# Kernel optimization log

Measured on AMD Instinct MI355X. Metric: run time of the kernel, lower is better.

Reference implementation:

```python
import jax, jax.numpy as jnp
import numpy as np

FIELD_DIMS = [100000, 1000, 100, 50]
NUM_FEATURES = 12
NUM_CAT = len(FIELD_DIMS)
NUM_CONT = NUM_FEATURES - NUM_CAT
D = 32            # embed_dim
HID = [64, 32]
B, T = 1024, 200
BN_EPS = 1e-5


def setup_inputs() -> dict:
    key = jax.random.key(0)
    ks = jax.random.split(key, 32)
    # x: [B, T, F]; first NUM_CAT cols are integer category ids stored as float
    cat_cols = [jax.random.randint(ks[i], (B, T, 1), 0, FIELD_DIMS[i]).astype(jnp.float32)
                for i in range(NUM_CAT)]
    cont_cols = jax.random.normal(ks[4], (B, T, NUM_CONT), dtype=jnp.float32)
    x = jnp.concatenate(cat_cols + [cont_cols], axis=-1)
    s = 0.05
    inp = {"x": x}
    for i, fd in enumerate(FIELD_DIMS):
        inp[f"emb{i}"] = jax.random.normal(ks[5 + i], (fd, D), dtype=jnp.float32) * s
        inp[f"lin{i}"] = jax.random.normal(ks[9 + i], (fd, D), dtype=jnp.float32) * s
    # Conv1d(1, D, 1) per continuous field == per-field affine map scalar -> D
    inp["cont_w"]  = jax.random.normal(ks[13], (NUM_CONT, D), dtype=jnp.float32) * s
    inp["cont_b"]  = jax.random.normal(ks[14], (NUM_CONT, D), dtype=jnp.float32) * s
    inp["clin_w"]  = jax.random.normal(ks[15], (NUM_CONT, D), dtype=jnp.float32) * s
    inp["clin_b"]  = jax.random.normal(ks[16], (NUM_CONT, D), dtype=jnp.float32) * s
    inp["fin_bias"] = jnp.zeros((D,), dtype=jnp.float32)
    # DNN tower: kernel_size-1 Conv1d == dense over channel dim
    dims = [NUM_FEATURES * D] + HID
    for li in range(len(HID)):
        fan_in = dims[li]
        inp[f"w{li+1}"] = jax.random.normal(ks[17 + 4 * li], (HID[li], fan_in), dtype=jnp.float32) / np.sqrt(fan_in)
        inp[f"b{li+1}"] = jnp.zeros((HID[li],), dtype=jnp.float32)
        inp[f"g{li+1}"] = jnp.ones((HID[li],), dtype=jnp.float32)
        inp[f"beta{li+1}"] = jnp.zeros((HID[li],), dtype=jnp.float32)
    inp["w_out"] = jax.random.normal(ks[30], (D, HID[-1]), dtype=jnp.float32) / np.sqrt(HID[-1])
    inp["b_out"] = jnp.zeros((D,), dtype=jnp.float32)
    return inp


def _batchnorm(h, g, b):
    # training-mode BN over (batch, time), biased variance (torch default)
    mu = h.mean(axis=(0, 1))
    var = h.var(axis=(0, 1))
    return g * (h - mu) * jax.lax.rsqrt(var + BN_EPS) + b


def reference(x, emb0, emb1, emb2, emb3, lin0, lin1, lin2, lin3,
              cont_w, cont_b, clin_w, clin_b, fin_bias,
              w1, b1, g1, beta1, w2, b2, g2, beta2, w_out, b_out):
    embs = [emb0, emb1, emb2, emb3]
    lins = [lin0, lin1, lin2, lin3]
    cat_idx = x[..., :NUM_CAT].astype(jnp.int32)          # [B,T,C]
    xc = x[..., NUM_CAT:]                                  # [B,T,Nc]

    # per-field embeddings -> [B,T,F,D]
    cat_emb = jnp.stack([embs[i][cat_idx[..., i]] for i in range(NUM_CAT)], axis=2)
    cont_emb = xc[..., None] * cont_w + cont_b             # [B,T,Nc,D]
    emb_all = jnp.concatenate([cat_emb, cont_emb], axis=2)  # [B,T,F,D]

    # FM pairwise interaction (sum-of-squares trick)
    s = emb_all.sum(axis=2)                                # [B,T,D]
    interaction = 0.5 * (s * s - (emb_all * emb_all).sum(axis=2))

    # linear terms
    lin_cat = sum(lins[i][cat_idx[..., i]] for i in range(NUM_CAT))      # [B,T,D]
    lin_cont = (xc[..., None] * clin_w + clin_b).sum(axis=2)             # [B,T,D]
    linear = lin_cat + lin_cont + fin_bias

    # DNN tower (k=1 convs == dense over F*D channels); dropout omitted (eval)
    h = emb_all.reshape(B, T, NUM_FEATURES * D)
    h = jax.nn.relu(_batchnorm(h @ w1.T + b1, g1, beta1))
    h = jax.nn.relu(_batchnorm(h @ w2.T + b2, g2, beta2))
    dnn = h @ w_out.T + b_out                              # [B,T,D]

    return linear + interaction + dnn                      # [B,T,D]
```

## Files before the change

kernel.cpp:

```cpp
#include <hip/hip_runtime.h>
#include <hip/hip_bf16.h>

typedef __hip_bfloat16 bf16;

#define ROWS 204800
#define N_INV (1.0f / 204800.0f)

__device__ float g_stats[256];
__device__ bf16  g_E1_0b[100000 * 64];
__device__ float g_E1_1[1000 * 64];
__device__ float g_E1_2[100 * 64];
__device__ float g_E1_3[50 * 64];
__device__ float g_U[8 * 64];
__device__ float g_Vb[64];
__device__ bf16  g_h1p[ROWS * 64];
__device__ bf16  g_h2p[ROWS * 32];
__device__ bf16  g_fmp[ROWS * 32];

__device__ __forceinline__ int clampi(int v, int hi) {
    return v < 0 ? 0 : (v > hi ? hi : v);
}
__device__ __forceinline__ float rl_f(float v, int l) {
    return __uint_as_float((unsigned int)__builtin_amdgcn_readlane((int)__float_as_uint(v), l));
}
__device__ __forceinline__ float us2f(unsigned short u) {
    return __uint_as_float(((unsigned int)u) << 16);
}

__global__ __launch_bounds__(64) void precompute_kernel(
    const float* __restrict__ emb1, const float* __restrict__ emb2, const float* __restrict__ emb3,
    const float* __restrict__ cont_w, const float* __restrict__ cont_b,
    const float* __restrict__ w1, const float* __restrict__ b1)
{
    int b = blockIdx.x;
    int k = threadIdx.x;
    __shared__ float row[32];

    if (b < 1150) {
        const float* tab; float* out; int i, colOff;
        if (b < 1000)      { tab = emb1; out = g_E1_1; i = b;        colOff = 32; }
        else if (b < 1100) { tab = emb2; out = g_E1_2; i = b - 1000; colOff = 64; }
        else               { tab = emb3; out = g_E1_3; i = b - 1100; colOff = 96; }
        if (k < 32) row[k] = tab[i * 32 + k];
        __syncthreads();
        const float* wr = w1 + k * 384 + colOff;
        float acc = 0.f;
        #pragma unroll
        for (int d = 0; d < 32; ++d) acc = fmaf(row[d], wr[d], acc);
        out[i * 64 + k] = acc;
    } else {
        g_stats[k]       = 0.f;
        g_stats[k + 64]  = 0.f;
        g_stats[k + 128] = 0.f;
        g_stats[k + 192] = 0.f;

        float vb = b1[k];
        #pragma unroll
        for (int j = 0; j < 8; ++j) {
            const float* wr = w1 + k * 384 + (4 + j) * 32;
            float u = 0.f;
            #pragma unroll
            for (int d = 0; d < 32; ++d) {
                float w = wr[d];
                u  = fmaf(cont_w[j * 32 + d], w, u);
                vb = fmaf(cont_b[j * 32 + d], w, vb);
            }
            g_U[j * 64 + k] = u;
        }
        g_Vb[k] = vb;
    }
}

__global__ __launch_bounds__(256) void e10_kernel(
    const float* __restrict__ emb0, const float* __restrict__ w1)
{
    int lane = threadIdx.x & 63;
    int wv   = threadIdx.x >> 6;
    int h    = lane >> 5;

    float w1col[32];
    {
        const float4* wr = (const float4*)(w1 + lane * 384);
        #pragma unroll
        for (int q = 0; q < 8; ++q) {
            float4 v = wr[q];
            w1col[4*q+0] = v.x; w1col[4*q+1] = v.y;
            w1col[4*q+2] = v.z; w1col[4*q+3] = v.w;
        }
    }

    for (int i = blockIdx.x * 8 + wv * 2; i < 100000; i += gridDim.x * 8) {
        int iA = i, iB = i + 1;
        float e = emb0[(h ? iB : iA) * 32 + (lane & 31)];

        float a0 = 0.f, a1 = 0.f, a2 = 0.f, a3 = 0.f;
        float b0 = 0.f, b1v = 0.f, b2v = 0.f, b3 = 0.f;
        #pragma unroll
        for (int dd = 0; dd < 32; dd += 4) {
            a0  = fmaf(rl_f(e, dd + 0),      w1col[dd + 0], a0);
            a1  = fmaf(rl_f(e, dd + 1),      w1col[dd + 1], a1);
            a2  = fmaf(rl_f(e, dd + 2),      w1col[dd + 2], a2);
            a3  = fmaf(rl_f(e, dd + 3),      w1col[dd + 3], a3);
            b0  = fmaf(rl_f(e, 32 + dd + 0), w1col[dd + 0], b0);
            b1v = fmaf(rl_f(e, 32 + dd + 1), w1col[dd + 1], b1v);
            b2v = fmaf(rl_f(e, 32 + dd + 2), w1col[dd + 2], b2v);
            b3  = fmaf(rl_f(e, 32 + dd + 3), w1col[dd + 3], b3);
        }
        g_E1_0b[iA * 64 + lane] = __float2bfloat16((a0 + a1) + (a2 + a3));
        g_E1_0b[iB * 64 + lane] = __float2bfloat16((b0 + b1v) + (b2v + b3));
    }
}

__global__ __launch_bounds__(256) void phase1_kernel(
    const float* __restrict__ x,
    const float* __restrict__ emb0, const float* __restrict__ lin0,
    const float* __restrict__ emb1, const float* __restrict__ lin1,
    const float* __restrict__ emb2, const float* __restrict__ lin2,
    const float* __restrict__ emb3, const float* __restrict__ lin3,
    const float* __restrict__ cont_w, const float* __restrict__ cont_b,
    const float* __restrict__ clin_w, const float* __restrict__ clin_b,
    const float* __restrict__ fin_bias)
{
    __shared__ float lsum[64], lsq[64];

    int tid  = threadIdx.x;
    int lane = tid & 63;
    int wv   = tid >> 6;
    int d    = lane & 31;
    bool lo  = lane < 32;

    if (tid < 64) { lsum[tid] = 0.f; lsq[tid] = 0.f; }
    __syncthreads();

    float uk[8];
    #pragma unroll
    for (int j = 0; j < 8; ++j) uk[j] = g_U[j * 64 + lane];
    float vbk = g_Vb[lane];

    float p1[8], p2[8], fb = 0.f;
    if (lo) {
        #pragma unroll
        for (int j = 0; j < 8; ++j) { p1[j] = cont_w[j * 32 + d]; p2[j] = cont_b[j * 32 + d]; }
    } else {
        #pragma unroll
        for (int j = 0; j < 8; ++j) { p1[j] = clin_w[j * 32 + d]; p2[j] = clin_b[j * 32 + d]; }
        fb = fin_bias[d];
    }

    const float* T0 = lo ? emb0 : lin0;
    const float* T1 = lo ? emb1 : lin1;
    const float* T2 = lo ? emb2 : lin2;
    const float* T3 = lo ? emb3 : lin3;

    int gw   = blockIdx.x * 4 + wv;
    int base = gw * 16;

    float xs[4];
    #pragma unroll
    for (int g = 0; g < 4; ++g)
        xs[g] = (lane < 48) ? x[(base + 4 * g) * 12 + lane] : 0.f;

    float ga[2][4], gb[2][4], gc[2][4], gd[2][4], t1[2][4], t2[2][4], t3[2][4];
    unsigned short e0u[2][4];

    auto issue = [&](int g, int s) {
        #pragma unroll
        for (int t = 0; t < 4; ++t) {
            int f  = t * 12;
            int i0 = clampi((int)rl_f(xs[g], f + 0), 99999);
            int i1 = clampi((int)rl_f(xs[g], f + 1), 999);
            int i2 = clampi((int)rl_f(xs[g], f + 2), 99);
            int i3 = clampi((int)rl_f(xs[g], f + 3), 49);
            ga[s][t]  = T0[i0 * 32 + d];
            gb[s][t]  = T1[i1 * 32 + d];
            gc[s][t]  = T2[i2 * 32 + d];
            gd[s][t]  = T3[i3 * 32 + d];
            e0u[s][t] = ((const unsigned short*)g_E1_0b)[i0 * 64 + lane];
            t1[s][t]  = g_E1_1[i1 * 64 + lane];
            t2[s][t]  = g_E1_2[i2 * 64 + lane];
            t3[s][t]  = g_E1_3[i3 * 64 + lane];
        }
    };

    issue(0, 0);

    float ss = 0.f, qq = 0.f;

    #pragma unroll
    for (int g = 0; g < 4; ++g) {
        int s = g & 1;
        if (g < 3) issue(g + 1, (g + 1) & 1);

        #pragma unroll
        for (int t = 0; t < 4; ++t) {
            int r  = base + 4 * g + t;
            int fo = t * 12 + 4;
            float xc[8];
            #pragma unroll
            for (int j = 0; j < 8; ++j) xc[j] = rl_f(xs[g], fo + j);

            float va = ga[s][t], vb = gb[s][t], vc = gc[s][t], vd = gd[s][t];

            float half_val;
            if (lo) {
                float s0 = va + vb, s1 = vc + vd;
                float q0 = fmaf(va, va, vb * vb);
                float q1 = fmaf(vc, vc, vd * vd);
                #pragma unroll
                for (int j = 0; j < 8; ++j) {
                    float ce = fmaf(xc[j], p1[j], p2[j]);
                    if (j & 1) { s1 += ce; q1 = fmaf(ce, ce, q1); }
                    else       { s0 += ce; q0 = fmaf(ce, ce, q0); }
                }
                float sfull = s0 + s1;
                half_val = 0.5f * (sfull * sfull - (q0 + q1));
            } else {
                float l0 = va + vb + fb, l1 = vc + vd;
                #pragma unroll
                for (int j = 0; j < 8; ++j) {
                    if (j & 1) l1 = fmaf(xc[j], p1[j], l1 + p2[j]);
                    else       l0 = fmaf(xc[j], p1[j], l0 + p2[j]);
                }
                half_val = l0 + l1;
            }
            float other = __shfl(half_val, lane | 32);
            if (lo) g_fmp[r * 32 + d] = __float2bfloat16(half_val + other);

            float h1 = ((vbk + us2f(e0u[s][t])) + (t1[s][t] + t2[s][t])) + t3[s][t];
            #pragma unroll
            for (int j = 0; j < 8; ++j) h1 = fmaf(xc[j], uk[j], h1);

            g_h1p[r * 64 + lane] = __float2bfloat16(h1);
            ss += h1;
            qq = fmaf(h1, h1, qq);
        }
    }

    atomicAdd(&lsum[lane], ss);
    atomicAdd(&lsq[lane], qq);
    __syncthreads();
    if (tid < 64) {
        atomicAdd(&g_stats[tid], lsum[tid]);
        atomicAdd(&g_stats[64 + tid], lsq[tid]);
    }
}

__global__ __launch_bounds__(256) void phase2_kernel(
    const float* __restrict__ w2, const float* __restrict__ b2,
    const float* __restrict__ g1, const float* __restrict__ beta1)
{
    __shared__ float sa[64], sc[64];
    __shared__ float ls[64];
    int tid  = threadIdx.x;
    if (tid < 64) {
        float mu  = g_stats[tid] * N_INV;
        float var = g_stats[64 + tid] * N_INV - mu * mu;
        float a   = g1[tid] * rsqrtf(var + 1e-5f);
        sa[tid] = a;
        sc[tid] = beta1[tid] - a * mu;
        ls[tid] = 0.f;
    }
    __syncthreads();

    int lane = tid & 63;
    int wv   = tid >> 6;
    size_t row = (size_t)(blockIdx.x * 4 + wv) * 64 + lane;

    const uint4* hrow = (const uint4*)(g_h1p + row * 64);

    float acc[32];
    #pragma unroll
    for (int m = 0; m < 32; ++m) acc[m] = 0.f;

    #pragma unroll
    for (int half = 0; half < 2; ++half) {
        uint4 u[4];
        #pragma unroll
        for (int q = 0; q < 4; ++q) u[q] = hrow[half * 4 + q];

        float y[32];
        #pragma unroll
        for (int q = 0; q < 4; ++q) {
            unsigned int w4[4] = {u[q].x, u[q].y, u[q].z, u[q].w};
            #pragma unroll
            for (int j = 0; j < 4; ++j) {
                int i  = q * 4 + j;
                int ch = half * 32 + 2 * i;
                float f0 = __uint_as_float(w4[j] << 16);
                float f1 = __uint_as_float(w4[j] & 0xffff0000u);
                y[2*i]     = fmaxf(0.f, fmaf(sa[ch],     f0, sc[ch]));
                y[2*i + 1] = fmaxf(0.f, fmaf(sa[ch + 1], f1, sc[ch + 1]));
            }
        }

        #pragma unroll
        for (int m = 0; m < 32; ++m) {
            const float* wr = w2 + m * 64 + half * 32;
            float a0 = 0.f, a1 = 0.f, a2 = 0.f, a3 = 0.f;
            #pragma unroll
            for (int k = 0; k < 32; k += 4) {
                a0 = fmaf(y[k + 0], wr[k + 0], a0);
                a1 = fmaf(y[k + 1], wr[k + 1], a1);
                a2 = fmaf(y[k + 2], wr[k + 2], a2);
                a3 = fmaf(y[k + 3], wr[k + 3], a3);
            }
            acc[m] += (a0 + a1) + (a2 + a3);
        }
    }

    #pragma unroll
    for (int m = 0; m < 32; ++m) acc[m] += b2[m];

    uint4 o[4];
    unsigned int* ow = (unsigned int*)o;
    #pragma unroll
    for (int i = 0; i < 16; ++i) {
        unsigned int lo16 = (unsigned int)__bfloat16_as_ushort(__float2bfloat16(acc[2*i]));
        unsigned int hi16 = (unsigned int)__bfloat16_as_ushort(__float2bfloat16(acc[2*i + 1]));
        ow[i] = lo16 | (hi16 << 16);
    }
    uint4* orow = (uint4*)(g_h2p + row * 32);
    #pragma unroll
    for (int q = 0; q < 4; ++q) orow[q] = o[q];

    #pragma unroll
    for (int c0 = 0; c0 < 32; c0 += 8) {
        float s[8], q[8];
        #pragma unroll
        for (int j = 0; j < 8; ++j) { s[j] = acc[c0 + j]; q[j] = s[j] * s[j]; }
        #pragma unroll
        for (int off = 32; off >= 1; off >>= 1) {
            #pragma unroll
            for (int j = 0; j < 8; ++j) {
                s[j] += __shfl_xor(s[j], off);
                q[j] += __shfl_xor(q[j], off);
            }
        }
        if (lane == 0) {
            #pragma unroll
            for (int j = 0; j < 8; ++j) {
                atomicAdd(&ls[c0 + j],      s[j]);
                atomicAdd(&ls[32 + c0 + j], q[j]);
            }
        }
    }
    __syncthreads();
    if (tid < 32)       atomicAdd(&g_stats[128 + tid], ls[tid]);
    else if (tid < 64)  atomicAdd(&g_stats[160 + (tid - 32)], ls[tid]);
}

__global__ __launch_bounds__(256) void phase3_kernel(
    const float* __restrict__ w_out, const float* __restrict__ b_out,
    const float* __restrict__ g2, const float* __restrict__ beta2,
    float* __restrict__ out)
{
    __shared__ float sa[32], sc[32];
    int tid  = threadIdx.x;
    if (tid < 32) {
        float mu  = g_stats[128 + tid] * N_INV;
        float var = g_stats[160 + tid] * N_INV - mu * mu;
        float a   = g2[tid] * rsqrtf(var + 1e-5f);
        sa[tid] = a;
        sc[tid] = beta2[tid] - a * mu;
    }
    __syncthreads();

    int lane = tid & 63;
    int wv   = tid >> 6;
    size_t row = (size_t)(blockIdx.x * 4 + wv) * 64 + lane;

    const uint4* hrow = (const uint4*)(g_h2p + row * 32);
    const uint4* frow = (const uint4*)(g_fmp + row * 32);
    uint4 u[4], fm4[4];
    #pragma unroll
    for (int q = 0; q < 4; ++q) { u[q] = hrow[q]; fm4[q] = frow[q]; }

    float y2[32];
    #pragma unroll
    for (int q = 0; q < 4; ++q) {
        unsigned int w4[4] = {u[q].x, u[q].y, u[q].z, u[q].w};
        #pragma unroll
        for (int j = 0; j < 4; ++j) {
            int i = q * 4 + j;
            float f0 = __uint_as_float(w4[j] << 16);
            float f1 = __uint_as_float(w4[j] & 0xffff0000u);
            y2[2*i]     = fmaxf(0.f, fmaf(sa[2*i],     f0, sc[2*i]));
            y2[2*i + 1] = fmaxf(0.f, fmaf(sa[2*i + 1], f1, sc[2*i + 1]));
        }
    }

    float fmv[32];
    {
        const unsigned int* fw = (const unsigned int*)fm4;
        #pragma unroll
        for (int i = 0; i < 16; ++i) {
            fmv[2*i]     = __uint_as_float(fw[i] << 16);
            fmv[2*i + 1] = __uint_as_float(fw[i] & 0xffff0000u);
        }
    }

    float res[32];
    #pragma unroll
    for (int dd = 0; dd < 32; ++dd) {
        const float* wr = w_out + dd * 32;
        float a0 = fmv[dd] + b_out[dd], a1 = 0.f, a2 = 0.f, a3 = 0.f;
        #pragma unroll
        for (int k = 0; k < 32; k += 4) {
            a0 = fmaf(y2[k + 0], wr[k + 0], a0);
            a1 = fmaf(y2[k + 1], wr[k + 1], a1);
            a2 = fmaf(y2[k + 2], wr[k + 2], a2);
            a3 = fmaf(y2[k + 3], wr[k + 3], a3);
        }
        res[dd] = (a0 + a1) + (a2 + a3);
    }

    float4* orow = (float4*)(out + row * 32);
    #pragma unroll
    for (int q = 0; q < 8; ++q)
        orow[q] = make_float4(res[4*q+0], res[4*q+1], res[4*q+2], res[4*q+3]);
}

extern "C" void kernel_launch(void* const* d_in, const int* in_sizes, int n_in,
                              void* d_out, int out_size, void* d_ws, size_t ws_size,
                              hipStream_t stream) {
    (void)in_sizes; (void)n_in; (void)out_size; (void)d_ws; (void)ws_size;

    const float* x       = (const float*)d_in[0];
    const float* emb0    = (const float*)d_in[1];
    const float* lin0    = (const float*)d_in[2];
    const float* emb1    = (const float*)d_in[3];
    const float* lin1    = (const float*)d_in[4];
    const float* emb2    = (const float*)d_in[5];
    const float* lin2    = (const float*)d_in[6];
    const float* emb3    = (const float*)d_in[7];
    const float* lin3    = (const float*)d_in[8];
    const float* cont_w  = (const float*)d_in[9];
    const float* cont_b  = (const float*)d_in[10];
    const float* clin_w  = (const float*)d_in[11];
    const float* clin_b  = (const float*)d_in[12];
    const float* fin_bias= (const float*)d_in[13];
    const float* w1      = (const float*)d_in[14];
    const float* b1      = (const float*)d_in[15];
    const float* g1      = (const float*)d_in[16];
    const float* beta1   = (const float*)d_in[17];
    const float* w2      = (const float*)d_in[18];
    const float* b2      = (const float*)d_in[19];
    const float* g2      = (const float*)d_in[20];
    const float* beta2   = (const float*)d_in[21];
    const float* w_out   = (const float*)d_in[22];
    const float* b_out   = (const float*)d_in[23];

    float* outp = (float*)d_out;

    hipLaunchKernelGGL(precompute_kernel, dim3(1151), dim3(64), 0, stream,
                       emb1, emb2, emb3, cont_w, cont_b, w1, b1);

    hipLaunchKernelGGL(e10_kernel, dim3(1600), dim3(256), 0, stream, emb0, w1);

    hipLaunchKernelGGL(phase1_kernel, dim3(3200), dim3(256), 0, stream,
                       x, emb0, lin0, emb1, lin1, emb2, lin2, emb3, lin3,
                       cont_w, cont_b, clin_w, clin_b, fin_bias);

    hipLaunchKernelGGL(phase2_kernel, dim3(800), dim3(256), 0, stream,
                       w2, b2, g1, beta1);

    hipLaunchKernelGGL(phase3_kernel, dim3(800), dim3(256), 0, stream,
                       w_out, b_out, g2, beta2, outp);
}
```

Baseline: 339.8 us.

## Stage phase2/phase3 row loads and stores through swizzled LDS for coalescing

Phase2 and phase3 previously had each lane read and write its own row with 16-byte strided accesses, which coalesce poorly across the wavefront. The kernels now use global_load_lds to bring each wave's 64-row tile into shared memory with an XOR swizzle that avoids bank conflicts. Outputs (h2 and the final result) are also staged through LDS, so global stores are contiguous across lanes. This costs extra LDS (32 KB per block), which can reduce occupancy. It also depends on hand-written waitcnt asm being correct, with no barrier between the wave-private LDS write and read.

```diff
diff --git a/kernel.cpp b/kernel.cpp
--- a/kernel.cpp
+++ b/kernel.cpp
@@ -26,6 +26,18 @@
 __device__ __forceinline__ float us2f(unsigned short u) {
     return __uint_as_float(((unsigned int)u) << 16);
 }
+
+__device__ __forceinline__ int swz8(int d) {
+    return (d & ~7) | ((d & 7) ^ ((d >> 3) & 7));
+}
+__device__ __forceinline__ int swz4(int d) {
+    return (d & ~3) | ((d & 3) ^ (((d >> 2) ^ (d >> 4)) & 3));
+}
+
+#define GLOAD16(gp, lp)                                                        \
+    __builtin_amdgcn_global_load_lds(                                          \
+        (const __attribute__((address_space(1))) unsigned int*)(gp),           \
+        (__attribute__((address_space(3))) unsigned int*)(lp), 16, 0, 0)
 
 __global__ __launch_bounds__(64) void precompute_kernel(
     const float* __restrict__ emb1, const float* __restrict__ emb2, const float* __restrict__ emb3,
@@ -251,7 +263,22 @@
 {
     __shared__ float sa[64], sc[64];
     __shared__ float ls[64];
+    __shared__ uint4 hbuf[4][512];
+
     int tid  = threadIdx.x;
+    int lane = tid & 63;
+    int wv   = tid >> 6;
+    size_t rowBase = (size_t)(blockIdx.x * 4 + wv) * 64;
+
+    {
+        const char* gsrc = (const char*)g_h1p + rowBase * 128;
+        #pragma unroll
+        for (int i = 0; i < 8; ++i) {
+            int dlin = (i << 6) + lane;
+            GLOAD16(gsrc + swz8(dlin) * 16, &hbuf[wv][i << 6]);
+        }
+    }
+
     if (tid < 64) {
         float mu  = g_stats[tid] * N_INV;
         float var = g_stats[64 + tid] * N_INV - mu * mu;
@@ -261,12 +288,10 @@
         ls[tid] = 0.f;
     }
     __syncthreads();
-
-    int lane = tid & 63;
-    int wv   = tid >> 6;
-    size_t row = (size_t)(blockIdx.x * 4 + wv) * 64 + lane;
-
-    const uint4* hrow = (const uint4*)(g_h1p + row * 64);
+    asm volatile("s_waitcnt vmcnt(0)" ::: "memory");
+
+    const uint4* lrow = hbuf[wv] + (lane << 3);
+    int r7 = lane & 7;
 
     float acc[32];
     #pragma unroll
@@ -276,7 +301,7 @@
     for (int half = 0; half < 2; ++half) {
         uint4 u[4];
         #pragma unroll
-        for (int q = 0; q < 4; ++q) u[q] = hrow[half * 4 + q];
+        for (int q = 0; q < 4; ++q) u[q] = lrow[(half * 4 + q) ^ r7];
 
         float y[32];
         #pragma unroll
@@ -319,9 +344,18 @@
         unsigned int hi16 = (unsigned int)__bfloat16_as_ushort(__float2bfloat16(acc[2*i + 1]));
         ow[i] = lo16 | (hi16 << 16);
     }
-    uint4* orow = (uint4*)(g_h2p + row * 32);
-    #pragma unroll
-    for (int q = 0; q < 4; ++q) orow[q] = o[q];
+
+    #pragma unroll
+    for (int q = 0; q < 4; ++q) hbuf[wv][swz4((lane << 2) + q)] = o[q];
+    asm volatile("s_waitcnt lgkmcnt(0)" ::: "memory");
+    {
+        uint4* og = (uint4*)(g_h2p + rowBase * 32);
+        #pragma unroll
+        for (int i = 0; i < 4; ++i) {
+            int dlin = (i << 6) + lane;
+            og[dlin] = hbuf[wv][swz4(dlin)];
+        }
+    }
 
     #pragma unroll
     for (int c0 = 0; c0 < 32; c0 += 8) {
@@ -355,7 +389,28 @@
     float* __restrict__ out)
 {
     __shared__ float sa[32], sc[32];
+    __shared__ uint4 sbuf[4][512];
+
     int tid  = threadIdx.x;
+    int lane = tid & 63;
+    int wv   = tid >> 6;
+    size_t rowBase = (size_t)(blockIdx.x * 4 + wv) * 64;
+
+    {
+        const char* gh2 = (const char*)g_h2p + rowBase * 64;
+        const char* gfm = (const char*)g_fmp + rowBase * 64;
+        #pragma unroll
+        for (int i = 0; i < 4; ++i) {
+            int dlin = (i << 6) + lane;
+            GLOAD16(gh2 + swz4(dlin) * 16, &sbuf[wv][i << 6]);
+        }
+        #pragma unroll
+        for (int i = 0; i < 4; ++i) {
+            int dlin = (i << 6) + lane;
+            GLOAD16(gfm + swz4(dlin) * 16, &sbuf[wv][256 + (i << 6)]);
+        }
+    }
+
     if (tid < 32) {
         float mu  = g_stats[128 + tid] * N_INV;
         float var = g_stats[160 + tid] * N_INV - mu * mu;
@@ -364,16 +419,15 @@
         sc[tid] = beta2[tid] - a * mu;
     }
     __syncthreads();
-
-    int lane = tid & 63;
-    int wv   = tid >> 6;
-    size_t row = (size_t)(blockIdx.x * 4 + wv) * 64 + lane;
-
-    const uint4* hrow = (const uint4*)(g_h2p + row * 32);
-    const uint4* frow = (const uint4*)(g_fmp + row * 32);
+    asm volatile("s_waitcnt vmcnt(0)" ::: "memory");
+
     uint4 u[4], fm4[4];
     #pragma unroll
-    for (int q = 0; q < 4; ++q) { u[q] = hrow[q]; fm4[q] = frow[q]; }
+    for (int q = 0; q < 4; ++q) {
+        int gidx = swz4((lane << 2) + q);
+        u[q]   = sbuf[wv][gidx];
+        fm4[q] = sbuf[wv][256 + gidx];
+    }
 
     float y2[32];
     #pragma unroll
@@ -414,10 +468,24 @@
         res[dd] = (a0 + a1) + (a2 + a3);
     }
 
-    float4* orow = (float4*)(out + row * 32);
-    #pragma unroll
-    for (int q = 0; q < 8; ++q)
-        orow[q] = make_float4(res[4*q+0], res[4*q+1], res[4*q+2], res[4*q+3]);
+    #pragma unroll
+    for (int q = 0; q < 8; ++q) {
+        uint4 v;
+        v.x = __float_as_uint(res[4*q+0]);
+        v.y = __float_as_uint(res[4*q+1]);
+        v.z = __float_as_uint(res[4*q+2]);
+        v.w = __float_as_uint(res[4*q+3]);
+        sbuf[wv][swz8((lane << 3) + q)] = v;
+    }
+    asm volatile("s_waitcnt lgkmcnt(0)" ::: "memory");
+    {
+        uint4* og = (uint4*)(out + rowBase * 32);
+        #pragma unroll
+        for (int i = 0; i < 8; ++i) {
+            int dlin = (i << 6) + lane;
+            og[dlin] = sbuf[wv][swz8(dlin)];
+        }
+    }
 }
 
 extern "C" void kernel_launch(void* const* d_in, const int* in_sizes, int n_in,
```

Measured after the change: 346.0 us. Within noise of the previous version (+1.8%).
